# Optimization experiments

Measured on AMD Instinct MI355X. Metric: run time of the kernel, lower is better.

## Reference

```python
import jax, jax.numpy as jnp
import numpy as np

T, B = 128, 256
E, H, C = 128, 1024, 10
VOCAB = 10


def setup_inputs() -> dict:
    key = jax.random.key(0)
    ks = jax.random.split(key, 12)
    x = jax.random.randint(ks[0], (T, B), 0, VOCAB)
    emb = jax.random.normal(ks[1], (VOCAB, E), dtype=jnp.float32)
    Wgx = jax.random.normal(ks[2], (E, H), dtype=jnp.float32) / np.sqrt(E)
    Wgh = jax.random.normal(ks[3], (H, H), dtype=jnp.float32) / np.sqrt(H)
    Wix = jax.random.normal(ks[4], (E, H), dtype=jnp.float32) / np.sqrt(E)
    Wih = jax.random.normal(ks[5], (H, H), dtype=jnp.float32) / np.sqrt(H)
    Wfx = jax.random.normal(ks[6], (E, H), dtype=jnp.float32) / np.sqrt(E)
    Wfh = jax.random.normal(ks[7], (H, H), dtype=jnp.float32) / np.sqrt(H)
    Wox = jax.random.normal(ks[8], (E, H), dtype=jnp.float32) / np.sqrt(E)
    Woh = jax.random.normal(ks[9], (H, H), dtype=jnp.float32) / np.sqrt(H)
    Wph = jax.random.normal(ks[10], (H, C), dtype=jnp.float32) / np.sqrt(H)
    bg = jnp.zeros((H,), jnp.float32)
    bi = jnp.zeros((H,), jnp.float32)
    bf = jnp.zeros((H,), jnp.float32)
    bo = jnp.zeros((H,), jnp.float32)
    bp = jnp.zeros((C,), jnp.float32)
    return dict(x=x, emb=emb, Wgx=Wgx, Wgh=Wgh, Wix=Wix, Wih=Wih, Wfx=Wfx,
                Wfh=Wfh, Wox=Wox, Woh=Woh, bg=bg, bi=bi, bf=bf, bo=bo,
                Wph=Wph, bp=bp)


def reference(x, emb, Wgx, Wgh, Wix, Wih, Wfx, Wfh, Wox, Woh,
              bg, bi, bf, bo, Wph, bp):
    Bsz = x.shape[1]
    Hn = Wgh.shape[0]
    # Fuse the 8 gate matmuls into 2 GEMMs per step (same math, concat order g,i,f,o)
    Wx = jnp.concatenate([Wgx, Wix, Wfx, Wox], axis=1)  # [E, 4H]
    Wh = jnp.concatenate([Wgh, Wih, Wfh, Woh], axis=1)  # [H, 4H]
    b = jnp.concatenate([bg, bi, bf, bo], axis=0)        # [4H]

    def step(carry, xt):
        state, hidden = carry
        e = emb[xt]                                      # [B, E]
        pre = e @ Wx + hidden @ Wh + b                   # [B, 4H]
        g = jnp.tanh(pre[:, :Hn])
        i = jax.nn.sigmoid(pre[:, Hn:2 * Hn])
        f = jax.nn.sigmoid(pre[:, 2 * Hn:3 * Hn])
        o = jax.nn.sigmoid(pre[:, 3 * Hn:])
        state = g * i + state * f
        hidden = jnp.tanh(state) * o
        return (state, hidden), None

    init = (jnp.zeros((Bsz, Hn), jnp.float32), jnp.zeros((Bsz, Hn), jnp.float32))
    (state, hidden), _ = jax.lax.scan(step, init, x)
    # Original detaches hidden/state before the output projection
    hidden = jax.lax.stop_gradient(hidden)
    return hidden @ Wph + bp                             # [B, C]
```

## Files before the change

kernel.cpp:

```cpp
#include <hip/hip_runtime.h>

typedef __bf16 bf16;
typedef __bf16 bf16x8 __attribute__((ext_vector_type(8)));
typedef float  f32x4  __attribute__((ext_vector_type(4)));
typedef int    i32x4  __attribute__((ext_vector_type(4)));

#define T_STEPS 128
#define BATCH   256
#define HD      1024
#define N4H     4096
#define EMB_D   128

#define MFMA_BF16(acc, Aop, Bop) \
    asm("v_mfma_f32_16x16x32_bf16 %0, %1, %2, %0" : "+v"(acc) : "a"(Aop), "v"(Bop))

__device__ __forceinline__ float fast_sigmoid(float x) {
    return 1.0f / (1.0f + __expf(-x));
}
__device__ __forceinline__ float fast_tanh(float x) {
    return 1.0f - 2.0f / (__expf(2.0f * x) + 1.0f);
}

__global__ void build_P(const float* __restrict__ emb,
                        const float* __restrict__ Wgx, const float* __restrict__ Wix,
                        const float* __restrict__ Wfx, const float* __restrict__ Wox,
                        const float* __restrict__ bg,  const float* __restrict__ bi,
                        const float* __restrict__ bfv, const float* __restrict__ bo,
                        float* __restrict__ P)
{
    int n = blockIdx.x * 256 + threadIdx.x;
    int v  = n >> 12;
    int nn = n & (N4H - 1);
    int hcol = nn >> 2, gate = nn & 3;
    const float* Wx = (gate == 0) ? Wgx : (gate == 1) ? Wix : (gate == 2) ? Wfx : Wox;
    const float* bb = (gate == 0) ? bg  : (gate == 1) ? bi  : (gate == 2) ? bfv : bo;
    float s = bb[hcol];
    for (int e = 0; e < EMB_D; ++e)
        s += emb[v * EMB_D + e] * Wx[e * HD + hcol];
    P[n] = s;
}

__global__ void build_W(const float* __restrict__ Wgh, const float* __restrict__ Wih,
                        const float* __restrict__ Wfh, const float* __restrict__ Woh,
                        bf16* __restrict__ WhpT)
{
    __shared__ float tile[64][65];
    int bid  = blockIdx.x;
    int gate = bid >> 8;
    int t2   = bid & 255;
    int kt = t2 >> 4, ht = t2 & 15;
    const float* W = (gate == 0) ? Wgh : (gate == 1) ? Wih : (gate == 2) ? Wfh : Woh;
    int tid = threadIdx.x;
    #pragma unroll
    for (int it = 0; it < 16; ++it) {
        int idx = it * 256 + tid;
        int kk = idx >> 6, hh = idx & 63;
        tile[kk][hh] = W[(size_t)(kt * 64 + kk) * HD + ht * 64 + hh];
    }
    __syncthreads();
    #pragma unroll
    for (int it = 0; it < 16; ++it) {
        int idx = it * 256 + tid;
        int hh = idx >> 6, kk = idx & 63;
        int n = (ht * 64 + hh) * 4 + gate;
        WhpT[(size_t)n * HD + kt * 64 + kk] = (bf16)tile[kk][hh];
    }
}

__global__ __launch_bounds__(512, 2)
void lstm_main(const int* __restrict__ x, const float* __restrict__ P,
               const bf16* __restrict__ WhpT, bf16* __restrict__ hbuf,
               int* __restrict__ ctl)
{
    __shared__ bf16  Blds[32][1024];
    __shared__ float red[8][64][9];
    __shared__ bf16  hst[32][34];

    const int tid  = threadIdx.x;
    const int lane = tid & 63;
    const int wid  = tid >> 6;
    const int w    = wid & 3;
    const int kh   = wid >> 2;
    const int frow = lane & 15;
    const int kgrp = lane >> 4;
    const int bid  = blockIdx.x;
    const int g    = bid & 7;
    const int j    = bid >> 3;

    int* bar = ctl + g * 16;

    const int rowO = j * 128 + w * 32 + kh * 16 + frow;
    const int rowX = j * 128 + w * 32 + (1 - kh) * 16 + frow;
    const bf16* AbO = WhpT + (size_t)rowO * HD + kh * 512 + kgrp * 8;
    const bf16* AbX = WhpT + (size_t)rowX * HD + kh * 512 + kgrp * 8;
    i32x4 ArO[16], ArX[16];
    #pragma unroll
    for (int ks = 0; ks < 16; ++ks) {
        ArO[ks] = *(const i32x4*)(const void*)(AbO + ks * 32);
        ArX[ks] = *(const i32x4*)(const void*)(AbX + ks * 32);
    }
    #pragma unroll
    for (int ks = 0; ks < 16; ++ks)
        asm volatile("" : "+a"(ArO[ks]), "+a"(ArX[ks]));

    const int mr0 = g * 32 + frow;
    const int clc = w * 8 + kh * 4 + kgrp;
    const int pnb = j * 128 + clc * 4;
    const int xorf = frow & 7;
    char* BB = (char*)&Blds[0][0];
    float* rw = &red[0][0][0] + ((size_t)(wid ^ 4) * 64 + lane) * 9;
    const float* rr = &red[0][0][0] + ((size_t)wid * 64 + lane) * 9;

    float st0 = 0.f, st1 = 0.f;
    f32x4 accP0, accP1;
    {
        int xv0 = x[mr0], xv1 = x[mr0 + 16];
        accP0 = *(const f32x4*)(P + (size_t)xv0 * N4H + pnb);
        accP1 = *(const f32x4*)(P + (size_t)xv1 * N4H + pnb);
    }

    for (int t = 0; t < T_STEPS; ++t) {
        f32x4 accO0 = accP0, accO1 = accP1;
        f32x4 z = {0.f, 0.f, 0.f, 0.f};
        f32x4 accX0 = z, accX1 = z;

        if (t > 0) {
            if (tid == 0) {
                const int tgt = 32 * t;
                long guard = 0;
                while (__hip_atomic_load(bar, __ATOMIC_RELAXED, __HIP_MEMORY_SCOPE_AGENT) < tgt
                       && ++guard < (1L << 24)) {}
            }
            __syncthreads();
            const char* src = (const char*)(hbuf + (size_t)(t & 1) * BATCH * HD
                                                 + (size_t)g * 32 * HD);
            f32x4 stg[8];
            #pragma unroll
            for (int i2 = 0; i2 < 8; ++i2)
                asm volatile("global_load_dwordx4 %0, %1, off sc0 sc1"
                             : "=v"(stg[i2]) : "v"(src + (i2 * 512 + tid) * 16));
            asm volatile("s_waitcnt vmcnt(0)" ::: "memory");
            #pragma unroll
            for (int i2 = 0; i2 < 8; ++i2) {
                int c = i2 * 512 + tid;
                int row = c >> 7, cg = c & 127;
                *(f32x4*)(BB + row * 2048 + ((cg ^ (row & 7)) << 4)) = stg[i2];
            }
            __syncthreads();
            #pragma unroll
            for (int ks = 0; ks < 16; ++ks) {
                int off = ((kh * 64 + ks * 4 + kgrp) ^ xorf) << 4;
                i32x4 b0 = *(const i32x4*)(BB + frow * 2048 + off);
                i32x4 b1 = *(const i32x4*)(BB + (frow + 16) * 2048 + off);
                MFMA_BF16(accO0, ArO[ks], b0);
                MFMA_BF16(accO1, ArO[ks], b1);
                MFMA_BF16(accX0, ArX[ks], b0);
                MFMA_BF16(accX1, ArX[ks], b1);
            }
        }

        rw[0] = accX0[0]; rw[1] = accX0[1]; rw[2] = accX0[2]; rw[3] = accX0[3];
        rw[4] = accX1[0]; rw[5] = accX1[1]; rw[6] = accX1[2]; rw[7] = accX1[3];
        __syncthreads();
        accO0[0] += rr[0]; accO0[1] += rr[1]; accO0[2] += rr[2]; accO0[3] += rr[3];
        accO1[0] += rr[4]; accO1[1] += rr[5]; accO1[2] += rr[6]; accO1[3] += rr[7];

        {
            float gg = fast_tanh(accO0[0]);
            float ii = fast_sigmoid(accO0[1]);
            float ff = fast_sigmoid(accO0[2]);
            float oo = fast_sigmoid(accO0[3]);
            float s = gg * ii + st0 * ff;
            st0 = s;
            hst[frow][clc] = (bf16)(fast_tanh(s) * oo);
        }
        {
            float gg = fast_tanh(accO1[0]);
            float ii = fast_sigmoid(accO1[1]);
            float ff = fast_sigmoid(accO1[2]);
            float oo = fast_sigmoid(accO1[3]);
            float s = gg * ii + st1 * ff;
            st1 = s;
            hst[frow + 16][clc] = (bf16)(fast_tanh(s) * oo);
        }

        if (t < T_STEPS - 1) {
            int xv0 = x[(t + 1) * BATCH + mr0], xv1 = x[(t + 1) * BATCH + mr0 + 16];
            accP0 = *(const f32x4*)(P + (size_t)xv0 * N4H + pnb);
            accP1 = *(const f32x4*)(P + (size_t)xv1 * N4H + pnb);
        }

        __syncthreads();
        {
            bf16* hout = hbuf + (size_t)((t + 1) & 1) * BATCH * HD;
            int r = tid >> 4, cp = (tid & 15) * 2;
            unsigned lo = (unsigned)__builtin_bit_cast(unsigned short, hst[r][cp]);
            unsigned hi = (unsigned)__builtin_bit_cast(unsigned short, hst[r][cp + 1]);
            unsigned pv = lo | (hi << 16);
            const bf16* hp = hout + (size_t)(g * 32 + r) * HD + j * 32 + cp;
            asm volatile("global_store_dword %0, %1, off sc0 sc1"
                         :: "v"(hp), "v"(pv) : "memory");
        }
        asm volatile("s_waitcnt vmcnt(0)" ::: "memory");
        __syncthreads();
        if (tid == 0 && t < T_STEPS - 1)
            __hip_atomic_fetch_add(bar, 1, __ATOMIC_RELAXED, __HIP_MEMORY_SCOPE_AGENT);
    }
}

__global__ void proj_out(const bf16* __restrict__ h, const float* __restrict__ Wph,
                         const float* __restrict__ bp, float* __restrict__ out)
{
    __shared__ float red[256][10];
    int b = blockIdx.x, tid = threadIdx.x;
    float acc[10];
    #pragma unroll
    for (int c = 0; c < 10; ++c) acc[c] = 0.f;
    for (int k = tid; k < HD; k += 256) {
        float hv = (float)h[(size_t)b * HD + k];
        #pragma unroll
        for (int c = 0; c < 10; ++c)
            acc[c] += hv * Wph[k * 10 + c];
    }
    #pragma unroll
    for (int c = 0; c < 10; ++c) red[tid][c] = acc[c];
    __syncthreads();
    for (int s = 128; s > 0; s >>= 1) {
        if (tid < s) {
            #pragma unroll
            for (int c = 0; c < 10; ++c) red[tid][c] += red[tid + s][c];
        }
        __syncthreads();
    }
    if (tid < 10) out[b * 10 + tid] = red[0][tid] + bp[tid];
}

extern "C" void kernel_launch(void* const* d_in, const int* in_sizes, int n_in,
                              void* d_out, int out_size, void* d_ws, size_t ws_size,
                              hipStream_t stream)
{
    const int*   x   = (const int*)  d_in[0];
    const float* emb = (const float*)d_in[1];
    const float* Wgx = (const float*)d_in[2];
    const float* Wgh = (const float*)d_in[3];
    const float* Wix = (const float*)d_in[4];
    const float* Wih = (const float*)d_in[5];
    const float* Wfx = (const float*)d_in[6];
    const float* Wfh = (const float*)d_in[7];
    const float* Wox = (const float*)d_in[8];
    const float* Woh = (const float*)d_in[9];
    const float* bg  = (const float*)d_in[10];
    const float* bi  = (const float*)d_in[11];
    const float* bfv = (const float*)d_in[12];
    const float* bo  = (const float*)d_in[13];
    const float* Wph = (const float*)d_in[14];
    const float* bp  = (const float*)d_in[15];

    char* ws = (char*)d_ws;
    bf16*  WhpT = (bf16*)ws;
    float* P    = (float*)(ws + 8388608);
    bf16*  hbuf = (bf16*)(ws + 8388608 + 163840);
    int*   ctl  = (int*)(ws + 8388608 + 163840 + 1048576);

    hipMemsetAsync(ctl, 0, 8 * 16 * sizeof(int), stream);
    build_P<<<160, 256, 0, stream>>>(emb, Wgx, Wix, Wfx, Wox, bg, bi, bfv, bo, P);
    build_W<<<1024, 256, 0, stream>>>(Wgh, Wih, Wfh, Woh, WhpT);

    void* args[] = { (void*)&x, (void*)&P, (void*)&WhpT, (void*)&hbuf, (void*)&ctl };
    hipLaunchCooperativeKernel((void*)lstm_main, dim3(256), dim3(512), args, 0, stream);

    proj_out<<<256, 256, 0, stream>>>(hbuf, Wph, bp, (float*)d_out);
}
```

Baseline: 635.8 us.

## Map batch groups to XCDs and shard per-group barrier counters

Each block reads its hardware XCC id and uses it as the batch group, then takes a slot j from a per-XCC atomic ticket, so the 32 blocks that exchange hidden state sit on the same XCD and share its L2. The per-group barrier counter is split across 8 padded slots that the waiter sums, which cuts contention on a single atomic. The hidden-state loads drop sc1 and the stores become plain stores with no explicit waitcnt, relying on same-XCD L2 coherence. This assumes blocks are spread evenly, 32 per XCC; if they are not, the group mapping breaks. The explicit store-completion wait before the release atomic is also removed, which risks ordering problems.

```diff
diff --git a/kernel.cpp b/kernel.cpp
--- a/kernel.cpp
+++ b/kernel.cpp
@@ -75,6 +75,7 @@
     __shared__ bf16  Blds[32][1024];
     __shared__ float red[8][64][9];
     __shared__ bf16  hst[32][34];
+    __shared__ int   sj;
 
     const int tid  = threadIdx.x;
     const int lane = tid & 63;
@@ -83,11 +84,16 @@
     const int kh   = wid >> 2;
     const int frow = lane & 15;
     const int kgrp = lane >> 4;
-    const int bid  = blockIdx.x;
-    const int g    = bid & 7;
-    const int j    = bid >> 3;
-
-    int* bar = ctl + g * 16;
+
+    int xcc;
+    asm("s_getreg_b32 %0, hwreg(HW_REG_XCC_ID)" : "=s"(xcc));
+    const int g = xcc & 7;
+    if (tid == 0)
+        sj = __hip_atomic_fetch_add(ctl + 1024 + g * 16, 1,
+                                    __ATOMIC_RELAXED, __HIP_MEMORY_SCOPE_AGENT) & 31;
+    __syncthreads();
+    const int j = sj;
+    int* bar = ctl + g * 128;
 
     const int rowO = j * 128 + w * 32 + kh * 16 + frow;
     const int rowX = j * 128 + w * 32 + (1 - kh) * 16 + frow;
@@ -128,8 +134,14 @@
             if (tid == 0) {
                 const int tgt = 32 * t;
                 long guard = 0;
-                while (__hip_atomic_load(bar, __ATOMIC_RELAXED, __HIP_MEMORY_SCOPE_AGENT) < tgt
-                       && ++guard < (1L << 24)) {}
+                int sum;
+                do {
+                    sum = 0;
+                    #pragma unroll
+                    for (int s8 = 0; s8 < 8; ++s8)
+                        sum += __hip_atomic_load(bar + s8 * 16, __ATOMIC_RELAXED,
+                                                 __HIP_MEMORY_SCOPE_AGENT);
+                } while (sum < tgt && ++guard < (1L << 22));
             }
             __syncthreads();
             const char* src = (const char*)(hbuf + (size_t)(t & 1) * BATCH * HD
@@ -137,7 +149,7 @@
             f32x4 stg[8];
             #pragma unroll
             for (int i2 = 0; i2 < 8; ++i2)
-                asm volatile("global_load_dwordx4 %0, %1, off sc0 sc1"
+                asm volatile("global_load_dwordx4 %0, %1, off sc0"
                              : "=v"(stg[i2]) : "v"(src + (i2 * 512 + tid) * 16));
             asm volatile("s_waitcnt vmcnt(0)" ::: "memory");
             #pragma unroll
@@ -197,14 +209,12 @@
             unsigned lo = (unsigned)__builtin_bit_cast(unsigned short, hst[r][cp]);
             unsigned hi = (unsigned)__builtin_bit_cast(unsigned short, hst[r][cp + 1]);
             unsigned pv = lo | (hi << 16);
-            const bf16* hp = hout + (size_t)(g * 32 + r) * HD + j * 32 + cp;
-            asm volatile("global_store_dword %0, %1, off sc0 sc1"
-                         :: "v"(hp), "v"(pv) : "memory");
-        }
-        asm volatile("s_waitcnt vmcnt(0)" ::: "memory");
+            *(unsigned*)(hout + (size_t)(g * 32 + r) * HD + j * 32 + cp) = pv;
+        }
         __syncthreads();
         if (tid == 0 && t < T_STEPS - 1)
-            __hip_atomic_fetch_add(bar, 1, __ATOMIC_RELAXED, __HIP_MEMORY_SCOPE_AGENT);
+            __hip_atomic_fetch_add(bar + (j & 7) * 16, 1,
+                                   __ATOMIC_RELAXED, __HIP_MEMORY_SCOPE_AGENT);
     }
 }
 
@@ -262,7 +272,7 @@
     bf16*  hbuf = (bf16*)(ws + 8388608 + 163840);
     int*   ctl  = (int*)(ws + 8388608 + 163840 + 1048576);
 
-    hipMemsetAsync(ctl, 0, 8 * 16 * sizeof(int), stream);
+    hipMemsetAsync(ctl, 0, 8192, stream);
     build_P<<<160, 256, 0, stream>>>(emb, Wgx, Wix, Wfx, Wox, bg, bi, bfv, bo, P);
     build_W<<<1024, 256, 0, stream>>>(Wgh, Wih, Wfh, Woh, WhpT);
 
```

After: 519.3 us (median of 2 runs). -18.3%, faster.
